# Kernel tuning notes

Hardware: AMD Instinct MI355X
Metric: run time of the kernel (lower is better)

The kernel has to match this reference:

```python
import jax, jax.numpy as jnp
import numpy as np

NUM_EMBEDDINGS = 512
EMBEDDING_DIM = 64


def setup_inputs() -> dict:
    key = jax.random.key(0)
    k1, k2 = jax.random.split(key)
    # latent from (identity) encoder, channels-last so view(-1, D) is valid
    z = jax.random.normal(k1, (32, 64, 64, EMBEDDING_DIM), dtype=jnp.float32)
    # codebook init: uniform(-1/K, 1/K) as in the torch module
    scale = 1.0 / NUM_EMBEDDINGS
    codebook = jax.random.uniform(
        k2, (NUM_EMBEDDINGS, EMBEDDING_DIM), dtype=jnp.float32,
        minval=-scale, maxval=scale)
    return {"z": z, "codebook": codebook}


def reference(z, codebook):
    # encoder = identity
    B, H, W, D = z.shape
    zf = z.reshape(-1, D)                                   # [N, D]
    # squared L2 distances: ||z||^2 + ||e||^2 - 2 z.e
    d = (jnp.sum(zf * zf, axis=1, keepdims=True)
         + jnp.sum(codebook * codebook, axis=1)
         - 2.0 * jnp.matmul(zf, codebook.T))                # [N, K]
    idx = jnp.argmin(d, axis=1)                             # [N]
    z_quantized = codebook[idx].reshape(z.shape)            # gather + reshape
    # decoder = identity
    x_recon = z_quantized
    return (x_recon, z_quantized)
```

## Files before the change

### kernel.cpp

```cpp
#include <hip/hip_runtime.h>
#include <math.h>

#define K_CODES 512
#define DIM 64
#define ROWS_PER_BLOCK 128
#define BROWS 512

__device__ __forceinline__ float np_pairwise_sumsq(const float* v) {
#pragma clang fp contract(off)
    float p[DIM];
#pragma unroll
    for (int j = 0; j < DIM; ++j) p[j] = v[j] * v[j];
    float r[8];
#pragma unroll
    for (int a = 0; a < 8; ++a) r[a] = p[a];
#pragma unroll
    for (int i = 8; i < DIM; i += 8) {
#pragma unroll
        for (int a = 0; a < 8; ++a) r[a] = r[a] + p[i + a];
    }
    return ((r[0] + r[1]) + (r[2] + r[3])) + ((r[4] + r[5]) + (r[6] + r[7]));
}

__device__ __forceinline__ float np_dot8acc(const float* zr, const float* ck) {
#pragma clang fp contract(off)
    float a0 = 0.f, a1 = 0.f, a2 = 0.f, a3 = 0.f;
    float a4 = 0.f, a5 = 0.f, a6 = 0.f, a7 = 0.f;
#pragma unroll
    for (int j = 0; j < DIM; j += 8) {
        a0 = fmaf(zr[j + 0], ck[j + 0], a0);
        a1 = fmaf(zr[j + 1], ck[j + 1], a1);
        a2 = fmaf(zr[j + 2], ck[j + 2], a2);
        a3 = fmaf(zr[j + 3], ck[j + 3], a3);
        a4 = fmaf(zr[j + 4], ck[j + 4], a4);
        a5 = fmaf(zr[j + 5], ck[j + 5], a5);
        a6 = fmaf(zr[j + 6], ck[j + 6], a6);
        a7 = fmaf(zr[j + 7], ck[j + 7], a7);
    }
    return ((a0 + a1) + (a2 + a3)) + ((a4 + a5) + (a6 + a7));
}

__global__ __launch_bounds__(256, 4) void vq_argmin_gather(
    const float* __restrict__ z, const float* __restrict__ cb,
    float* __restrict__ out, int n_rows) {
#pragma clang fp contract(off)
    __shared__ float esq_lds[K_CODES];
    __shared__ float red_d[ROWS_PER_BLOCK];
    __shared__ int   red_b[ROWS_PER_BLOCK];
    __shared__ int   best_lds[ROWS_PER_BLOCK];

    const int t = threadIdx.x;
    const int tr  = t & (ROWS_PER_BLOCK - 1);
    const int row = blockIdx.x * ROWS_PER_BLOCK + tr;
    const int k0 = __builtin_amdgcn_readfirstlane((t >> 7) << 8);

    float zr[DIM];
    const float4* zp = (const float4*)(z + (size_t)row * DIM);
#pragma unroll
    for (int j = 0; j < DIM / 4; ++j) {
        float4 v = zp[j];
        zr[4 * j + 0] = v.x; zr[4 * j + 1] = v.y;
        zr[4 * j + 2] = v.z; zr[4 * j + 3] = v.w;
    }
#pragma unroll
    for (int j = 0; j < DIM; ++j) { asm volatile("" : "+v"(zr[j])); }

    for (int c = t; c < K_CODES; c += 256)
        esq_lds[c] = np_pairwise_sumsq(cb + (size_t)c * DIM);
    __syncthreads();

    const float zsq = np_pairwise_sumsq(zr);
    float dmin = INFINITY;
    int best = k0;
    const float* __restrict__ cbase = cb + (size_t)k0 * DIM;
#pragma unroll 2
    for (int kk = 0; kk < K_CODES / 2; ++kk) {
        const float dot = np_dot8acc(zr, cbase + (size_t)kk * DIM);
        const float tkv = zsq + esq_lds[k0 + kk];
        const float m = 2.0f * dot;
        const float d = tkv - m;
        if (d < dmin) { dmin = d; best = k0 + kk; }
    }
    if (t >= ROWS_PER_BLOCK) { red_d[tr] = dmin; red_b[tr] = best; }
    __syncthreads();
    if (t < ROWS_PER_BLOCK) {
        int b = (red_d[tr] < dmin) ? red_b[tr] : best;
        best_lds[tr] = b;
    }
    __syncthreads();

    const float4* cb4 = (const float4*)cb;
    float4* o = (float4*)out;
    const size_t out1_off = (size_t)n_rows * (DIM / 4);
    const size_t grow = (size_t)blockIdx.x * ROWS_PER_BLOCK * (DIM / 4);
#pragma unroll
    for (int i = t; i < ROWS_PER_BLOCK * (DIM / 4); i += 256) {
        const int r = i >> 4;
        const int j = i & 15;
        const float4 v = cb4[(size_t)best_lds[r] * (DIM / 4) + j];
        const size_t g = grow + (size_t)r * (DIM / 4) + j;
        o[g] = v;
        o[g + out1_off] = v;
    }
}

typedef __bf16 bfx8 __attribute__((ext_vector_type(8)));
typedef float  f32x4 __attribute__((ext_vector_type(4)));

#define EPS_GAP 3.0e-5f

__device__ __forceinline__ void split_bf16(float x, unsigned short& h, unsigned short& l) {
    unsigned int xb = __float_as_uint(x);
    unsigned int hb = (xb + 0x8000u) & 0xffff0000u;
    h = (unsigned short)(hb >> 16);
    float lf = x - __uint_as_float(hb);
    l = (unsigned short)((__float_as_uint(lf) + 0x8000u) >> 16);
}

__global__ __launch_bounds__(1024)
__attribute__((amdgpu_waves_per_eu(4, 4))) void vq_fused(
    const float* __restrict__ z, const float* __restrict__ cb,
    float* __restrict__ out, int n_rows) {
#pragma clang fp contract(off)
    __shared__ unsigned short b_lds[K_CODES * DIM * 2];
    __shared__ float esq_lds[K_CODES];
    __shared__ int   best_lds[BROWS];
    __shared__ int   flaglist[BROWS];
    __shared__ float fd[16][64];
    __shared__ int   fk[16][64];
    __shared__ int   nflag;

    const int t = threadIdx.x;
    const int wave = t >> 6;
    const int lane = t & 63;
    const int lg = lane >> 4;
    const int lr = lane & 15;
    const int rb = blockIdx.x * BROWS;
    const int wrb = rb + wave * 32;

    if (t == 0) nflag = 0;

#pragma unroll
    for (int i = 0; i < 4; ++i) {
        const int id = t + i * 1024;
        const int l = id & 63;
        const int s = (id >> 6) & 1;
        const int tile = id >> 7;
        const int code = tile * 16 + (l & 15);
        const int d0 = s * 32 + (l >> 4) * 8;
        const float* p = cb + (size_t)code * DIM + d0;
        float4 v0 = *(const float4*)p;
        float4 v1 = *(const float4*)(p + 4);
        float f[8] = {v0.x, v0.y, v0.z, v0.w, v1.x, v1.y, v1.z, v1.w};
        union { unsigned short u[8]; uint4 q; } H, L;
#pragma unroll
        for (int j = 0; j < 8; ++j) split_bf16(f[j], H.u[j], L.u[j]);
        *(uint4*)(b_lds + (size_t)id * 8) = H.q;
        *(uint4*)(b_lds + 32768 + (size_t)id * 8) = L.q;
    }
    if (t < K_CODES) esq_lds[t] = np_pairwise_sumsq(cb + (size_t)t * DIM);

    bfx8 a_hi[2][2], a_lo[2][2];
#pragma unroll
    for (int RS = 0; RS < 2; ++RS) {
#pragma unroll
        for (int s = 0; s < 2; ++s) {
            const float* zp = z + (size_t)(wrb + RS * 16 + lr) * DIM + s * 32 + lg * 8;
            float4 v0 = *(const float4*)zp;
            float4 v1 = *(const float4*)(zp + 4);
            float f[8] = {v0.x, v0.y, v0.z, v0.w, v1.x, v1.y, v1.z, v1.w};
            union { unsigned short u[8]; bfx8 b; } H, L;
#pragma unroll
            for (int j = 0; j < 8; ++j) split_bf16(f[j], H.u[j], L.u[j]);
            a_hi[RS][s] = H.b;
            a_lo[RS][s] = L.b;
        }
    }
    __syncthreads();

    float b1[2][4], b2[2][4];
    int   k1[2][4];
#pragma unroll
    for (int RS = 0; RS < 2; ++RS)
#pragma unroll
        for (int i = 0; i < 4; ++i) { b1[RS][i] = INFINITY; b2[RS][i] = INFINITY; k1[RS][i] = 0; }

    for (int tt = 0; tt < 32; ++tt) {
        const int s0 = ((tt * 2 + 0) * 64 + lane) * 8;
        const int s1 = ((tt * 2 + 1) * 64 + lane) * 8;
        bfx8 bh0 = *(const bfx8*)(b_lds + s0);
        bfx8 bh1 = *(const bfx8*)(b_lds + s1);
        bfx8 bl0 = *(const bfx8*)(b_lds + 32768 + s0);
        bfx8 bl1 = *(const bfx8*)(b_lds + 32768 + s1);

        f32x4 acc0 = {0.f, 0.f, 0.f, 0.f};
        f32x4 acc1 = {0.f, 0.f, 0.f, 0.f};
        acc0 = __builtin_amdgcn_mfma_f32_16x16x32_bf16(a_hi[0][0], bh0, acc0, 0, 0, 0);
        acc0 = __builtin_amdgcn_mfma_f32_16x16x32_bf16(a_hi[0][1], bh1, acc0, 0, 0, 0);
        acc0 = __builtin_amdgcn_mfma_f32_16x16x32_bf16(a_hi[0][0], bl0, acc0, 0, 0, 0);
        acc0 = __builtin_amdgcn_mfma_f32_16x16x32_bf16(a_hi[0][1], bl1, acc0, 0, 0, 0);
        acc0 = __builtin_amdgcn_mfma_f32_16x16x32_bf16(a_lo[0][0], bh0, acc0, 0, 0, 0);
        acc0 = __builtin_amdgcn_mfma_f32_16x16x32_bf16(a_lo[0][1], bh1, acc0, 0, 0, 0);
        acc1 = __builtin_amdgcn_mfma_f32_16x16x32_bf16(a_hi[1][0], bh0, acc1, 0, 0, 0);
        acc1 = __builtin_amdgcn_mfma_f32_16x16x32_bf16(a_hi[1][1], bh1, acc1, 0, 0, 0);
        acc1 = __builtin_amdgcn_mfma_f32_16x16x32_bf16(a_hi[1][0], bl0, acc1, 0, 0, 0);
        acc1 = __builtin_amdgcn_mfma_f32_16x16x32_bf16(a_hi[1][1], bl1, acc1, 0, 0, 0);
        acc1 = __builtin_amdgcn_mfma_f32_16x16x32_bf16(a_lo[1][0], bh0, acc1, 0, 0, 0);
        acc1 = __builtin_amdgcn_mfma_f32_16x16x32_bf16(a_lo[1][1], bh1, acc1, 0, 0, 0);

        const float ev = esq_lds[tt * 16 + lr];
        const int   kk = tt * 16 + lr;
#pragma unroll
        for (int i = 0; i < 4; ++i) {
            {
                float s = fmaf(-2.0f, acc0[i], ev);
                b2[0][i] = fminf(fmaxf(s, b1[0][i]), b2[0][i]);
                bool c = s < b1[0][i];
                b1[0][i] = c ? s : b1[0][i];
                k1[0][i] = c ? kk : k1[0][i];
            }
            {
                float s = fmaf(-2.0f, acc1[i], ev);
                b2[1][i] = fminf(fmaxf(s, b1[1][i]), b2[1][i]);
                bool c = s < b1[1][i];
                b1[1][i] = c ? s : b1[1][i];
                k1[1][i] = c ? kk : k1[1][i];
            }
        }
    }

#pragma unroll
    for (int m = 1; m <= 8; m <<= 1) {
#pragma unroll
        for (int RS = 0; RS < 2; ++RS) {
#pragma unroll
            for (int i = 0; i < 4; ++i) {
                float ob1 = __shfl_xor(b1[RS][i], m);
                int   ok1 = __shfl_xor(k1[RS][i], m);
                float ob2 = __shfl_xor(b2[RS][i], m);
                float nb2 = fminf(fmaxf(b1[RS][i], ob1), fminf(b2[RS][i], ob2));
                bool take = (ob1 < b1[RS][i]) || (ob1 == b1[RS][i] && ok1 < k1[RS][i]);
                b1[RS][i] = take ? ob1 : b1[RS][i];
                k1[RS][i] = take ? ok1 : k1[RS][i];
                b2[RS][i] = nb2;
            }
        }
    }

    if (lr == 0) {
#pragma unroll
        for (int RS = 0; RS < 2; ++RS) {
#pragma unroll
            for (int i = 0; i < 4; ++i) {
                const int rl = wave * 32 + RS * 16 + lg * 4 + i;
                best_lds[rl] = k1[RS][i];
                if (b2[RS][i] - b1[RS][i] <= EPS_GAP) {
                    int p = atomicAdd(&nflag, 1);
                    flaglist[p] = rl;
                }
            }
        }
    }
    __syncthreads();

    const int nf = nflag;
    for (int base = 0; base < nf; base += 64) {
        const bool active = (base + lane) < nf;
        const int rl = flaglist[active ? (base + lane) : base];
        const float* zp = z + (size_t)(rb + rl) * DIM;
        float zs[DIM];
#pragma unroll
        for (int j = 0; j < DIM / 4; ++j) {
            float4 v = ((const float4*)zp)[j];
            zs[4 * j + 0] = v.x; zs[4 * j + 1] = v.y;
            zs[4 * j + 2] = v.z; zs[4 * j + 3] = v.w;
        }
        const float zsq = np_pairwise_sumsq(zs);

        const int c0 = wave * 32;
        const float* cbase = cb + (size_t)c0 * DIM;
        float dmin = INFINITY;
        int bk = c0;
        for (int c = 0; c < 32; ++c) {
            const float dot = np_dot8acc(zs, cbase + (size_t)c * DIM);
            const float tkv = zsq + esq_lds[c0 + c];
            const float m2 = 2.0f * dot;
            const float d = tkv - m2;
            if (d < dmin) { dmin = d; bk = c0 + c; }
        }
        fd[wave][lane] = dmin;
        fk[wave][lane] = bk;
        __syncthreads();
        if (t < 64 && (base + t) < nf) {
            float d = fd[0][t];
            int   k = fk[0][t];
#pragma unroll
            for (int w = 1; w < 16; ++w) {
                float od = fd[w][t];
                int   ok = fk[w][t];
                bool take = (od < d) || (od == d && ok < k);
                d = take ? od : d;
                k = take ? ok : k;
            }
            best_lds[flaglist[base + t]] = k;
        }
        __syncthreads();
    }

    const float4* cb4 = (const float4*)cb;
    float4* o = (float4*)out;
    const size_t out1_off = (size_t)n_rows * (DIM / 4);
    const size_t grow = (size_t)blockIdx.x * BROWS * (DIM / 4);
#pragma unroll
    for (int i = t; i < BROWS * (DIM / 4); i += 1024) {
        const int r = i >> 4;
        const int j = i & 15;
        const float4 v = cb4[(size_t)best_lds[r] * (DIM / 4) + j];
        const size_t g = grow + (size_t)r * (DIM / 4) + j;
        o[g] = v;
        o[g + out1_off] = v;
    }
}

extern "C" void kernel_launch(void* const* d_in, const int* in_sizes, int n_in,
                              void* d_out, int out_size, void* d_ws, size_t ws_size,
                              hipStream_t stream) {
    const float* z  = (const float*)d_in[0];
    const float* cb = (const float*)d_in[1];
    float* out = (float*)d_out;

    const int n_rows = in_sizes[0] / DIM;

    if ((n_rows % BROWS) == 0) {
        vq_fused<<<dim3(n_rows / BROWS), dim3(1024), 0, stream>>>(z, cb, out, n_rows);
    } else {
        vq_argmin_gather<<<dim3(n_rows / ROWS_PER_BLOCK), dim3(256), 0, stream>>>(
            z, cb, out, n_rows);
    }
}
```

Measured before the change: 188.8 us.

## Move near-tie exact rescoring into a separate global fixup kernel

The per-block in-kernel fp32 rescoring of ambiguous rows (small top-2 gap) is removed from the main bf16-split MFMA kernel. Flagged rows are now appended to a global list through a global atomic counter, and a second kernel spreads the exact rescoring across many blocks, with each wave scanning 128 codes. The aim is to remove the load imbalance and block-wide barriers that flagged rows caused in the main kernel. In exchange it adds a memset, a second launch, global atomics, and a rewrite of the output for the flagged rows.

```diff
diff --git a/kernel.cpp b/kernel.cpp
--- a/kernel.cpp
+++ b/kernel.cpp
@@ -118,17 +118,14 @@
 }
 
 __global__ __launch_bounds__(1024)
-__attribute__((amdgpu_waves_per_eu(4, 4))) void vq_fused(
+__attribute__((amdgpu_waves_per_eu(4, 4))) void vq_main16(
     const float* __restrict__ z, const float* __restrict__ cb,
-    float* __restrict__ out, int n_rows) {
-#pragma clang fp contract(off)
+    float* __restrict__ out,
+    float* __restrict__ esq_ws, int* __restrict__ gcnt, int* __restrict__ grows,
+    int n_rows) {
     __shared__ unsigned short b_lds[K_CODES * DIM * 2];
     __shared__ float esq_lds[K_CODES];
     __shared__ int   best_lds[BROWS];
-    __shared__ int   flaglist[BROWS];
-    __shared__ float fd[16][64];
-    __shared__ int   fk[16][64];
-    __shared__ int   nflag;
 
     const int t = threadIdx.x;
     const int wave = t >> 6;
@@ -137,8 +134,6 @@
     const int lr = lane & 15;
     const int rb = blockIdx.x * BROWS;
     const int wrb = rb + wave * 32;
-
-    if (t == 0) nflag = 0;
 
 #pragma unroll
     for (int i = 0; i < 4; ++i) {
@@ -158,7 +153,11 @@
         *(uint4*)(b_lds + (size_t)id * 8) = H.q;
         *(uint4*)(b_lds + 32768 + (size_t)id * 8) = L.q;
     }
-    if (t < K_CODES) esq_lds[t] = np_pairwise_sumsq(cb + (size_t)t * DIM);
+    if (t < K_CODES) {
+        const float e = np_pairwise_sumsq(cb + (size_t)t * DIM);
+        esq_lds[t] = e;
+        if (blockIdx.x == 0) esq_ws[t] = e;
+    }
 
     bfx8 a_hi[2][2], a_lo[2][2];
 #pragma unroll
@@ -255,57 +254,13 @@
                 const int rl = wave * 32 + RS * 16 + lg * 4 + i;
                 best_lds[rl] = k1[RS][i];
                 if (b2[RS][i] - b1[RS][i] <= EPS_GAP) {
-                    int p = atomicAdd(&nflag, 1);
-                    flaglist[p] = rl;
+                    int p = atomicAdd(gcnt, 1);
+                    grows[p] = rb + rl;
                 }
             }
         }
     }
     __syncthreads();
-
-    const int nf = nflag;
-    for (int base = 0; base < nf; base += 64) {
-        const bool active = (base + lane) < nf;
-        const int rl = flaglist[active ? (base + lane) : base];
-        const float* zp = z + (size_t)(rb + rl) * DIM;
-        float zs[DIM];
-#pragma unroll
-        for (int j = 0; j < DIM / 4; ++j) {
-            float4 v = ((const float4*)zp)[j];
-            zs[4 * j + 0] = v.x; zs[4 * j + 1] = v.y;
-            zs[4 * j + 2] = v.z; zs[4 * j + 3] = v.w;
-        }
-        const float zsq = np_pairwise_sumsq(zs);
-
-        const int c0 = wave * 32;
-        const float* cbase = cb + (size_t)c0 * DIM;
-        float dmin = INFINITY;
-        int bk = c0;
-        for (int c = 0; c < 32; ++c) {
-            const float dot = np_dot8acc(zs, cbase + (size_t)c * DIM);
-            const float tkv = zsq + esq_lds[c0 + c];
-            const float m2 = 2.0f * dot;
-            const float d = tkv - m2;
-            if (d < dmin) { dmin = d; bk = c0 + c; }
-        }
-        fd[wave][lane] = dmin;
-        fk[wave][lane] = bk;
-        __syncthreads();
-        if (t < 64 && (base + t) < nf) {
-            float d = fd[0][t];
-            int   k = fk[0][t];
-#pragma unroll
-            for (int w = 1; w < 16; ++w) {
-                float od = fd[w][t];
-                int   ok = fk[w][t];
-                bool take = (od < d) || (od == d && ok < k);
-                d = take ? od : d;
-                k = take ? ok : k;
-            }
-            best_lds[flaglist[base + t]] = k;
-        }
-        __syncthreads();
-    }
 
     const float4* cb4 = (const float4*)cb;
     float4* o = (float4*)out;
@@ -322,6 +277,85 @@
     }
 }
 
+__global__ __launch_bounds__(256, 1) void vq_fixup3(
+    const float* __restrict__ z, const float* __restrict__ cb,
+    const float* __restrict__ esq_g,
+    const int* __restrict__ gcnt, const int* __restrict__ grows,
+    float* __restrict__ out, int n_rows) {
+#pragma clang fp contract(off)
+    __shared__ float fd[4][64];
+    __shared__ int   fk[4][64];
+    __shared__ int   rowbuf[64];
+    __shared__ int   bestk[64];
+
+    const int t = threadIdx.x;
+    const int w = t >> 6;
+    const int lane = t & 63;
+    const int nf = gcnt[0];
+
+    for (int base = blockIdx.x * 64; base < nf; base += gridDim.x * 64) {
+        const int nvalid = min(64, nf - base);
+        if (t < 64) rowbuf[t] = grows[base + min(t, nvalid - 1)];
+        __syncthreads();
+
+        const int row = rowbuf[lane];
+        float zs[DIM];
+        const float4* zp = (const float4*)(z + (size_t)row * DIM);
+#pragma unroll
+        for (int j = 0; j < DIM / 4; ++j) {
+            float4 v = zp[j];
+            zs[4 * j + 0] = v.x; zs[4 * j + 1] = v.y;
+            zs[4 * j + 2] = v.z; zs[4 * j + 3] = v.w;
+        }
+        const float zsq = np_pairwise_sumsq(zs);
+
+        const int c0 = __builtin_amdgcn_readfirstlane(w * 128);
+        const float* cbase = cb + (size_t)c0 * DIM;
+        float dmin = INFINITY;
+        int bk = c0;
+        for (int c = 0; c < 128; ++c) {
+            const float dot = np_dot8acc(zs, cbase + (size_t)c * DIM);
+            const float tkv = zsq + esq_g[c0 + c];
+            const float m2 = 2.0f * dot;
+            const float d = tkv - m2;
+            if (d < dmin) { dmin = d; bk = c0 + c; }
+        }
+        fd[w][lane] = dmin;
+        fk[w][lane] = bk;
+        __syncthreads();
+
+        if (t < 64) {
+            float d = fd[0][t];
+            int   k = fk[0][t];
+#pragma unroll
+            for (int ww = 1; ww < 4; ++ww) {
+                float od = fd[ww][t];
+                int   ok = fk[ww][t];
+                bool take = (od < d) || (od == d && ok < k);
+                d = take ? od : d;
+                k = take ? ok : k;
+            }
+            bestk[t] = k;
+        }
+        __syncthreads();
+
+        const float4* cb4 = (const float4*)cb;
+        float4* o = (float4*)out;
+        const size_t out1_off = (size_t)n_rows * (DIM / 4);
+        for (int i = t; i < 64 * (DIM / 4); i += 256) {
+            const int r = i >> 4;
+            const int j = i & 15;
+            if (r < nvalid) {
+                const float4 v = cb4[(size_t)bestk[r] * (DIM / 4) + j];
+                const size_t g = (size_t)rowbuf[r] * (DIM / 4) + j;
+                o[g] = v;
+                o[g + out1_off] = v;
+            }
+        }
+        __syncthreads();
+    }
+}
+
 extern "C" void kernel_launch(void* const* d_in, const int* in_sizes, int n_in,
                               void* d_out, int out_size, void* d_ws, size_t ws_size,
                               hipStream_t stream) {
@@ -331,8 +365,16 @@
 
     const int n_rows = in_sizes[0] / DIM;
 
-    if ((n_rows % BROWS) == 0) {
-        vq_fused<<<dim3(n_rows / BROWS), dim3(1024), 0, stream>>>(z, cb, out, n_rows);
+    const size_t WS_NEED = 16 + K_CODES * 4 + (size_t)n_rows * 4;
+    if (ws_size >= WS_NEED && (n_rows % BROWS) == 0) {
+        int* gcnt = (int*)d_ws;
+        float* esq = (float*)(gcnt + 4);
+        int* grows = (int*)(esq + K_CODES);
+        hipMemsetAsync(gcnt, 0, 4, stream);
+        vq_main16<<<dim3(n_rows / BROWS), dim3(1024), 0, stream>>>(
+            z, cb, out, esq, gcnt, grows, n_rows);
+        vq_fixup3<<<dim3(1024), dim3(256), 0, stream>>>(
+            z, cb, esq, gcnt, grows, out, n_rows);
     } else {
         vq_argmin_gather<<<dim3(n_rows / ROWS_PER_BLOCK), dim3(256), 0, stream>>>(
             z, cb, out, n_rows);
```

Result: faster. 169.6 us (-10.1%).

## Rework flagged-row fallback to one wave per row with shuffle argmin

Applied to the files above, without the earlier changes.

The exact fp32 recheck for rows whose bf16 top-2 gap is small now assigns one flagged row per wave. The row is staged in LDS, and each lane scans 8 codes before a wave-level xor-shuffle argmin. This replaces the old scheme, where each lane owned a row and scanned 32 codes per wave, then combined results across waves through LDS with two block-wide barriers per batch. The aim is to cut the barriers and per-lane register pressure in the fallback. The trade-offs are broadcast LDS reads, uncoalesced per-lane codebook reads, and a different summation order for the squared norm, which could change tie-breaking slightly.

```diff
diff --git a/kernel.cpp b/kernel.cpp
--- a/kernel.cpp
+++ b/kernel.cpp
@@ -18,6 +18,19 @@
     for (int i = 8; i < DIM; i += 8) {
 #pragma unroll
         for (int a = 0; a < 8; ++a) r[a] = r[a] + p[i + a];
+    }
+    return ((r[0] + r[1]) + (r[2] + r[3])) + ((r[4] + r[5]) + (r[6] + r[7]));
+}
+
+__device__ __forceinline__ float np_pairwise_sumsq_chunked(const float* v) {
+#pragma clang fp contract(off)
+    float r[8];
+#pragma unroll
+    for (int a = 0; a < 8; ++a) r[a] = v[a] * v[a];
+#pragma unroll
+    for (int i = 8; i < DIM; i += 8) {
+#pragma unroll
+        for (int a = 0; a < 8; ++a) r[a] = r[a] + v[i + a] * v[i + a];
     }
     return ((r[0] + r[1]) + (r[2] + r[3])) + ((r[4] + r[5]) + (r[6] + r[7]));
 }
@@ -118,16 +131,14 @@
 }
 
 __global__ __launch_bounds__(1024)
-__attribute__((amdgpu_waves_per_eu(4, 4))) void vq_fused(
+__attribute__((amdgpu_waves_per_eu(4, 4))) void vq_fused2(
     const float* __restrict__ z, const float* __restrict__ cb,
     float* __restrict__ out, int n_rows) {
-#pragma clang fp contract(off)
     __shared__ unsigned short b_lds[K_CODES * DIM * 2];
     __shared__ float esq_lds[K_CODES];
     __shared__ int   best_lds[BROWS];
-    __shared__ int   flaglist[BROWS];
-    __shared__ float fd[16][64];
-    __shared__ int   fk[16][64];
+    __shared__ int   flag_lds[BROWS];
+    __shared__ float zlds[16][DIM];
     __shared__ int   nflag;
 
     const int t = threadIdx.x;
@@ -256,56 +267,50 @@
                 best_lds[rl] = k1[RS][i];
                 if (b2[RS][i] - b1[RS][i] <= EPS_GAP) {
                     int p = atomicAdd(&nflag, 1);
-                    flaglist[p] = rl;
+                    flag_lds[p] = rl;
                 }
             }
         }
     }
     __syncthreads();
 
-    const int nf = nflag;
-    for (int base = 0; base < nf; base += 64) {
-        const bool active = (base + lane) < nf;
-        const int rl = flaglist[active ? (base + lane) : base];
-        const float* zp = z + (size_t)(rb + rl) * DIM;
-        float zs[DIM];
-#pragma unroll
-        for (int j = 0; j < DIM / 4; ++j) {
-            float4 v = ((const float4*)zp)[j];
-            zs[4 * j + 0] = v.x; zs[4 * j + 1] = v.y;
-            zs[4 * j + 2] = v.z; zs[4 * j + 3] = v.w;
-        }
-        const float zsq = np_pairwise_sumsq(zs);
-
-        const int c0 = wave * 32;
-        const float* cbase = cb + (size_t)c0 * DIM;
-        float dmin = INFINITY;
-        int bk = c0;
-        for (int c = 0; c < 32; ++c) {
-            const float dot = np_dot8acc(zs, cbase + (size_t)c * DIM);
-            const float tkv = zsq + esq_lds[c0 + c];
-            const float m2 = 2.0f * dot;
-            const float d = tkv - m2;
-            if (d < dmin) { dmin = d; bk = c0 + c; }
-        }
-        fd[wave][lane] = dmin;
-        fk[wave][lane] = bk;
-        __syncthreads();
-        if (t < 64 && (base + t) < nf) {
-            float d = fd[0][t];
-            int   k = fk[0][t];
-#pragma unroll
-            for (int w = 1; w < 16; ++w) {
-                float od = fd[w][t];
-                int   ok = fk[w][t];
-                bool take = (od < d) || (od == d && ok < k);
-                d = take ? od : d;
-                k = take ? ok : k;
-            }
-            best_lds[flaglist[base + t]] = k;
-        }
-        __syncthreads();
-    }
+    const int nfl = nflag;
+    for (int base = 0; base < nfl; base += 16) {
+        const int idx = base + wave;
+        if (idx < nfl) {
+#pragma clang fp contract(off)
+            const int rl = flag_lds[idx];
+            const int row = rb + rl;
+            if (lane < 16) {
+                ((float4*)&zlds[wave][0])[lane] =
+                    ((const float4*)(z + (size_t)row * DIM))[lane];
+            }
+            asm volatile("s_waitcnt lgkmcnt(0) vmcnt(0)" ::: "memory");
+            const float* zp = (const float*)&zlds[wave][0];
+            const float zsq = np_pairwise_sumsq_chunked(zp);
+            float dmin = INFINITY;
+            int bk = lane * 8;
+            const float* cbase = cb + (size_t)(lane * 8) * DIM;
+#pragma unroll
+            for (int c = 0; c < 8; ++c) {
+                const float dot = np_dot8acc(zp, cbase + (size_t)c * DIM);
+                const float tkv = zsq + esq_lds[lane * 8 + c];
+                const float m2 = 2.0f * dot;
+                const float d = tkv - m2;
+                if (d < dmin) { dmin = d; bk = lane * 8 + c; }
+            }
+#pragma unroll
+            for (int m = 1; m <= 32; m <<= 1) {
+                float od = __shfl_xor(dmin, m);
+                int   ob = __shfl_xor(bk, m);
+                bool take = (od < dmin) || (od == dmin && ob < bk);
+                dmin = take ? od : dmin;
+                bk = take ? ob : bk;
+            }
+            if (lane == 0) best_lds[rl] = bk;
+        }
+    }
+    __syncthreads();
 
     const float4* cb4 = (const float4*)cb;
     float4* o = (float4*)out;
@@ -332,7 +337,7 @@
     const int n_rows = in_sizes[0] / DIM;
 
     if ((n_rows % BROWS) == 0) {
-        vq_fused<<<dim3(n_rows / BROWS), dim3(1024), 0, stream>>>(z, cb, out, n_rows);
+        vq_fused2<<<dim3(n_rows / BROWS), dim3(1024), 0, stream>>>(z, cb, out, n_rows);
     } else {
         vq_argmin_gather<<<dim3(n_rows / ROWS_PER_BLOCK), dim3(256), 0, stream>>>(
             z, cb, out, n_rows);
```

Result: faster. 163.5 us (-13.4%).
